# Kernel tuning notes

Measured on AMD Instinct MI355X. Metric: run time of the kernel, lower is better.

Reference implementation:

```python
import jax, jax.numpy as jnp
import numpy as np

K = 9          # neighbors per node (loop=False)
BN_EPS = 1e-5  # BatchNorm2d eps


def setup_inputs() -> dict:
    key = jax.random.key(0)
    k1, k2, k3 = jax.random.split(key, 3)
    B, C, H, W_ = 16, 384, 32, 32
    x = jax.random.normal(k1, (B, C, H, W_), dtype=jnp.float32)
    # GCNConv linear weight (PyG stores [out, in]; y = x @ W.T) and bias
    Wg = jax.random.normal(k2, (C, C), dtype=jnp.float32) / np.sqrt(C)
    bg = jax.random.normal(k3, (C,), dtype=jnp.float32) * 0.02
    gamma = jnp.ones((C,), dtype=jnp.float32)
    beta = jnp.zeros((C,), dtype=jnp.float32)
    return {"x": x, "Wg": Wg, "bg": bg, "gamma": gamma, "beta": beta}


def _knn_indices(xn):
    # xn: [B, N, C] -> neighbor indices [B, N, K] (self excluded)
    sq = jnp.sum(xn * xn, axis=-1)                       # [B, N]
    d = sq[:, :, None] + sq[:, None, :] - 2.0 * jnp.einsum("bnc,bmc->bnm", xn, xn)
    N = xn.shape[1]
    d = d + jnp.eye(N, dtype=xn.dtype) * jnp.finfo(xn.dtype).max  # exclude self
    _, nbr = jax.lax.top_k(-d, K)                        # [B, N, K]
    return nbr


def reference(x, Wg, bg, gamma, beta):
    B, C, H, W_ = x.shape
    N = H * W_
    BN_nodes = B * N
    shortcut = x

    # Flatten to nodes: [B*N, C]
    xn = jnp.transpose(x, (0, 2, 3, 1)).reshape(B, N, C)

    # Per-graph kNN in feature space (PyG knn_graph, flow source_to_target:
    # edges from neighbor (src) to query node (dst))
    nbr = _knn_indices(xn)                                # [B, N, K]
    offs = (jnp.arange(B) * N)[:, None, None]             # [B,1,1]
    src = (nbr + offs).reshape(-1)                        # [B*N*K]
    dst = jnp.broadcast_to(jnp.arange(N)[None, :, None] + offs, (B, N, K)).reshape(-1)

    # GCNConv: add self loops, symmetric normalization
    loops = jnp.arange(BN_nodes)
    src = jnp.concatenate([src, loops])
    dst = jnp.concatenate([dst, loops])

    xw = xn.reshape(BN_nodes, C) @ Wg.T                   # node-wise linear

    deg = jax.ops.segment_sum(jnp.ones_like(dst, dtype=xw.dtype), dst, num_segments=BN_nodes)
    dinv = jax.lax.rsqrt(deg)                             # deg >= 1 due to self loops
    norm = dinv[src] * dinv[dst]                          # [E]

    out = jax.ops.segment_sum(norm[:, None] * xw[src], dst, num_segments=BN_nodes) + bg

    # Back to B x C x H x W
    out = jnp.transpose(out.reshape(B, H, W_, C), (0, 3, 1, 2))

    # BatchNorm2d (training-mode batch statistics, biased variance)
    mu = jnp.mean(out, axis=(0, 2, 3), keepdims=True)
    var = jnp.mean((out - mu) ** 2, axis=(0, 2, 3), keepdims=True)
    out = gamma[None, :, None, None] * (out - mu) * jax.lax.rsqrt(var + BN_EPS) + beta[None, :, None, None]

    # GELU + residual (drop_path = 0 -> identity)
    out = jax.nn.gelu(out) + shortcut
    return out
```

## Files before the change

kernel.cpp:

```cpp
#include <hip/hip_runtime.h>
#include <math.h>

#define B_ 16
#define C_ 384
#define N_ 1024
#define K_ 9

typedef _Float16 f16x8 __attribute__((ext_vector_type(8)));
typedef _Float16 f16x4 __attribute__((ext_vector_type(4)));
typedef float f32x4 __attribute__((ext_vector_type(4)));
typedef unsigned long long u64;

__device__ __forceinline__ void gld_lds16(const void* g, void* l) {
  __builtin_amdgcn_global_load_lds((const __attribute__((address_space(1))) void*)g,
                                   (__attribute__((address_space(3))) void*)l, 16, 0, 0);
}

__global__ __launch_bounds__(256) void k_cvt(const float* __restrict__ x,
                                             const float* __restrict__ Wg,
                                             ushort* __restrict__ xhT, ushort* __restrict__ xlT,
                                             float* __restrict__ sq, ushort* __restrict__ WgH,
                                             ushort* __restrict__ WgL,
                                             float* __restrict__ stats) {
  const int bid = blockIdx.x;
  const int t = threadIdx.x;
  if (bid >= 512) {
    const int i = ((bid - 512) * 256 + t) * 4;
    float4 v = *(const float4*)(Wg + i);
    float vv[4] = {v.x, v.y, v.z, v.w};
    f16x4 hv, lv;
#pragma unroll
    for (int j = 0; j < 4; ++j) {
      _Float16 h = (_Float16)vv[j];
      hv[j] = h;
      lv[j] = (_Float16)(vv[j] - (float)h);
    }
    *(f16x4*)(WgH + i) = hv;
    *(f16x4*)(WgL + i) = lv;
    if (bid == 512) {
      stats[t] = 0.f;
      stats[t + 256] = 0.f;
      stats[t + 512] = 0.f;
    }
    return;
  }
  const int b = bid >> 5, n0 = (bid & 31) * 32;
  __shared__ float ld[384 * 33];
  {
    const int cb = t >> 2, j8 = (t & 3) * 8;
#pragma unroll
    for (int i = 0; i < 6; ++i) {
      const int c = i * 64 + cb;
      const float* src = x + ((size_t)(b * C_ + c) * N_ + n0 + j8);
      float4 v0 = *(const float4*)src;
      float4 v1 = *(const float4*)(src + 4);
      float* dst = &ld[c * 33 + j8];
      dst[0] = v0.x; dst[1] = v0.y; dst[2] = v0.z; dst[3] = v0.w;
      dst[4] = v1.x; dst[5] = v1.y; dst[6] = v1.z; dst[7] = v1.w;
    }
  }
  __syncthreads();
  {
    const int n = t >> 3, l = t & 7;
#pragma unroll
    for (int i = 0; i < 6; ++i) {
      const int c8 = i * 64 + l * 8;
      f16x8 hv, lv;
#pragma unroll
      for (int j = 0; j < 8; ++j) {
        float v = ld[(c8 + j) * 33 + n];
        _Float16 h = (_Float16)v;
        hv[j] = h;
        lv[j] = (_Float16)(v - (float)h);
      }
      const size_t off = (size_t)(b * N_ + n0 + n) * C_ + c8;
      *(f16x8*)(xhT + off) = hv;
      *(f16x8*)(xlT + off) = lv;
    }
    double s = 0.0;
    const int cbase = l * 48;
#pragma unroll
    for (int cc = 0; cc < 48; ++cc) {
      float v = ld[(cbase + cc) * 33 + n];
      s = fma((double)v, (double)v, s);
    }
    s += __shfl_xor(s, 1, 64);
    s += __shfl_xor(s, 2, 64);
    s += __shfl_xor(s, 4, 64);
    if (l == 0) sq[b * N_ + n0 + n] = (float)s;
  }
}

__device__ __forceinline__ void ce2f(float& a, float& b) {
  float lo = fminf(a, b), hi = fmaxf(a, b);
  a = lo;
  b = hi;
}
__device__ __forceinline__ void ce9u(u64& a, u64& b) {
  u64 lo = a < b ? a : b;
  u64 hi = a < b ? b : a;
  a = lo;
  b = hi;
}
__device__ __forceinline__ void mrg9(float* a, const float* b) {
  float m[9];
#pragma unroll
  for (int k = 0; k < 9; ++k) m[k] = fminf(a[k], b[8 - k]);
  ce2f(m[0], m[8]);
  ce2f(m[1], m[5]); ce2f(m[2], m[6]); ce2f(m[3], m[7]); ce2f(m[4], m[8]);
  ce2f(m[1], m[3]); ce2f(m[2], m[4]); ce2f(m[5], m[7]); ce2f(m[6], m[8]);
  ce2f(m[1], m[2]); ce2f(m[3], m[4]); ce2f(m[5], m[6]); ce2f(m[7], m[8]);
#pragma unroll
  for (int k = 0; k < 9; ++k) a[k] = m[k];
}

__global__ __launch_bounds__(256, 2) void k_gram(const ushort* __restrict__ xhT,
                                                 const ushort* __restrict__ xlT,
                                                 const float* __restrict__ sq,
                                                 u64* __restrict__ part, int base_b, int nb) {
  const int bid = blockIdx.x;
  int b_local, pid;
  if (nb >= 8) {
    const int x = bid & 7, j = bid >> 3, grp = nb >> 3;
    b_local = x * grp + (j >> 6);
    pid = j & 63;
  } else {
    b_local = bid >> 6;
    pid = bid & 63;
  }
  const int b = base_b + b_local;
  const int rt = pid >> 3, mt = pid & 7;
  const int n0 = rt * 128, m0 = mt * 128;

  __shared__ alignas(16) char sm[2][32768];
  const int t = threadIdx.x;
  const int lane = t & 63, wid = t >> 6, quad = lane >> 4, lrow = lane & 15;
  const int wr = wid >> 1, wc = wid & 1;
  const int lrow4 = lane >> 2, lpos = lane & 3;

  const char* src = (const char*)((wid & 1) ? xlT : xhT) +
                    (size_t)(b * N_ + ((wid >> 1) ? m0 : n0)) * C_ * 2;

  f32x4 acc[4][4];
#pragma unroll
  for (int mi = 0; mi < 4; ++mi)
#pragma unroll
    for (int ni = 0; ni < 4; ++ni) acc[mi][ni] = (f32x4){0.f, 0.f, 0.f, 0.f};

  auto stage = [&](int it) {
    char* dst = sm[it & 1] + wid * 8192;
    const int ktB = it * 64;
#pragma unroll
    for (int i = 0; i < 8; ++i) {
      const int row = i * 16 + lrow4;
      const int swz = lpos ^ ((row >> 1) & 3);
      gld_lds16(src + (size_t)row * 768 + ktB + swz * 16, dst + i * 1024 + lane * 16);
    }
  };

  stage(0);
  for (int it = 0; it < 12; ++it) {
    __syncthreads();
    if (it < 11) stage(it + 1);
    const char* smb = sm[it & 1];
    f16x8 ah[4], al[4];
#pragma unroll
    for (int mi = 0; mi < 4; ++mi) {
      const int row = wr * 64 + mi * 16 + lrow;
      const int off = row * 64 + (quad ^ ((row >> 1) & 3)) * 16;
      ah[mi] = *(const f16x8*)(smb + off);
      al[mi] = *(const f16x8*)(smb + 8192 + off);
    }
#pragma unroll
    for (int ni = 0; ni < 4; ++ni) {
      const int row = wc * 64 + ni * 16 + lrow;
      const int off = row * 64 + (quad ^ ((row >> 1) & 3)) * 16;
      f16x8 bh = *(const f16x8*)(smb + 16384 + off);
      f16x8 bl = *(const f16x8*)(smb + 24576 + off);
#pragma unroll
      for (int mi = 0; mi < 4; ++mi) {
        acc[mi][ni] = __builtin_amdgcn_mfma_f32_16x16x32_f16(bh, ah[mi], acc[mi][ni], 0, 0, 0);
        acc[mi][ni] = __builtin_amdgcn_mfma_f32_16x16x32_f16(bh, al[mi], acc[mi][ni], 0, 0, 0);
        acc[mi][ni] = __builtin_amdgcn_mfma_f32_16x16x32_f16(bl, ah[mi], acc[mi][ni], 0, 0, 0);
      }
    }
  }
  __syncthreads();

  const float* sqb = sq + b * N_;
  float sqm_[4][4];
#pragma unroll
  for (int ni = 0; ni < 4; ++ni)
#pragma unroll
    for (int r = 0; r < 4; ++r) sqm_[ni][r] = sqb[m0 + wc * 64 + ni * 16 + quad * 4 + r];
  float sqq_[4];
#pragma unroll
  for (int mi = 0; mi < 4; ++mi) sqq_[mi] = sqb[n0 + wr * 64 + mi * 16 + lrow];

  float* smf = (float*)sm;
#pragma unroll
  for (int mi = 0; mi < 4; ++mi) {
    const int qL = wr * 64 + mi * 16 + lrow;
    const int qG = n0 + qL;
#pragma unroll
    for (int ni = 0; ni < 4; ++ni) {
      const int tc = wc * 16 + ni * 4 + quad;
      const int stv = tc ^ (qL & 31);
      f32x4 dv;
#pragma unroll
      for (int r = 0; r < 4; ++r) {
        const int mG = m0 + wc * 64 + ni * 16 + quad * 4 + r;
        float d = fmaf(-2.f, acc[mi][ni][r], sqq_[mi] + sqm_[ni][r]);
        if (mG == qG) d = 3.402823466e38f;
        dv[r] = d;
      }
      *(f32x4*)(smf + qL * 128 + stv * 4) = dv;
    }
  }
  __syncthreads();

  const int qsel = wid * 32 + (lane & 31);
  const int half = lane >> 5;
  float kA[9], kB[9], kC[9], kD[9];
#pragma unroll
  for (int k = 0; k < 9; ++k) kA[k] = kB[k] = kC[k] = kD[k] = 3.402823466e38f;

  auto ins16 = [&](float* key, int tcb) {
#pragma unroll
    for (int i = 0; i < 4; ++i) {
      const int tc = tcb + i;
      const int stv = tc ^ (qsel & 31);
      f32x4 q4 = *(const f32x4*)(smf + qsel * 128 + stv * 4);
#pragma unroll
      for (int e = 0; e < 4; ++e) {
        key[8] = fminf(key[8], q4[e]);
#pragma unroll
        for (int s = 8; s >= 1; --s) ce2f(key[s - 1], key[s]);
      }
    }
  };
  ins16(kA, half * 16 + 0);
  ins16(kB, half * 16 + 4);
  ins16(kC, half * 16 + 8);
  ins16(kD, half * 16 + 12);
  mrg9(kA, kB);
  mrg9(kC, kD);
  mrg9(kA, kC);
  {
    float pk[9];
#pragma unroll
    for (int k = 0; k < 9; ++k) pk[k] = __shfl_xor(kA[k], 32, 64);
    float m[9];
#pragma unroll
    for (int k = 0; k < 9; ++k) m[k] = fminf(kA[k], pk[8 - k]);
    ce2f(m[0], m[8]);
    ce2f(m[1], m[5]); ce2f(m[2], m[6]); ce2f(m[3], m[7]); ce2f(m[4], m[8]);
    ce2f(m[1], m[3]); ce2f(m[2], m[4]); ce2f(m[5], m[7]); ce2f(m[6], m[8]);
    ce2f(m[1], m[2]); ce2f(m[3], m[4]); ce2f(m[5], m[6]); ce2f(m[7], m[8]);
#pragma unroll
    for (int k = 0; k < 9; ++k) kA[k] = m[k];
  }
  const float v9 = kA[8];
  int c_lt = 0;
#pragma unroll
  for (int k = 0; k < 8; ++k) c_lt += (kA[k] < v9) ? 1 : 0;

  u64 lt_mask = 0ull, eq_mask = 0ull;
#pragma unroll
  for (int i = 0; i < 16; ++i) {
    const int tc = half * 16 + i;
    const int stv = tc ^ (qsel & 31);
    f32x4 q4 = *(const f32x4*)(smf + qsel * 128 + stv * 4);
#pragma unroll
    for (int e = 0; e < 4; ++e) {
      const int j = i * 4 + e;
      lt_mask |= (q4[e] < v9) ? (1ull << j) : 0ull;
      eq_mask |= (q4[e] == v9) ? (1ull << j) : 0ull;
    }
  }
  const int ltc = __popcll(lt_mask), eqc = __popcll(eq_mask);
  const int packed = ltc | (eqc << 16);
  const int other = __shfl_xor(packed, 32, 64);
  const int lt_pref = half ? (other & 0xFFFF) : 0;
  const int eq_pref = half ? (other >> 16) : 0;

  u64* pp = part + (((size_t)(b_local * 8 + mt) * N_) + (n0 + qsel)) * 9;
  int slot = lt_pref;
  u64 msk = lt_mask;
  while (msk) {
    const int j = __builtin_ctzll(msk);
    msk &= msk - 1;
    const int mL = half * 64 + j;
    const int stv = (mL >> 2) ^ (qsel & 31);
    const float val = smf[qsel * 128 + stv * 4 + (mL & 3)];
    unsigned fb = __float_as_uint(val);
    unsigned mono = (fb >> 31) ? ~fb : (fb | 0x80000000u);
    pp[slot++] = ((u64)mono << 32) | (unsigned)(m0 + mL);
  }
  unsigned fb9 = __float_as_uint(v9);
  unsigned mono9 = (fb9 >> 31) ? ~fb9 : (fb9 | 0x80000000u);
  slot = c_lt + eq_pref;
  msk = eq_mask;
  while (msk && slot < 9) {
    const int j = __builtin_ctzll(msk);
    msk &= msk - 1;
    pp[slot++] = ((u64)mono9 << 32) | (unsigned)(m0 + half * 64 + j);
  }
}

__global__ void k_mrg(const u64* __restrict__ part, int* __restrict__ nbr, int base_node) {
  const int nl = blockIdx.x * 256 + threadIdx.x;
  const int bl = nl >> 10, q = nl & 1023;
  const u64* p = part + ((size_t)(bl * 8) * N_ + q) * 9;
  u64 key[9];
#pragma unroll
  for (int k = 0; k < 9; ++k) key[k] = ~0ull;
#pragma unroll
  for (int seg = 0; seg < 8; ++seg) {
    const u64* ps = p + (size_t)seg * N_ * 9;
#pragma unroll
    for (int k9 = 0; k9 < 9; ++k9) {
      u64 kk = ps[k9];
      key[8] = key[8] < kk ? key[8] : kk;
#pragma unroll
      for (int s = 8; s >= 1; --s) ce9u(key[s - 1], key[s]);
    }
  }
  int* np = nbr + (size_t)(base_node + nl) * K_;
#pragma unroll
  for (int k = 0; k < 9; ++k) np[k] = (int)(unsigned)(key[k] & 0xFFFFFFFFu);
}

__global__ __launch_bounds__(256, 3) void k_xw(const ushort* __restrict__ xhT,
                                               const ushort* __restrict__ xlT,
                                               const ushort* __restrict__ WgH,
                                               const ushort* __restrict__ WgL,
                                               float* __restrict__ xw) {
  const int bid = blockIdx.x;
  const int xcd = bid & 7, j = bid >> 3;
  const int pair = xcd * 16 + j / 6;
  const int ct = j % 6;
  const int b = pair >> 3, nt = pair & 7;
  const int co0 = ct * 64, n0 = nt * 128;
  __shared__ alignas(16) char sm[2][24576];
  const int t = threadIdx.x;
  const int lane = t & 63, wid = t >> 6, quad = lane >> 4, lrow = lane & 15;
  const int wr = wid >> 1, wc = wid & 1;
  const int lrow4 = lane >> 2, lpos = lane & 3;

  f32x4 acc[2][4];
#pragma unroll
  for (int mi = 0; mi < 2; ++mi)
#pragma unroll
    for (int ni = 0; ni < 4; ++ni) acc[mi][ni] = (f32x4){0.f, 0.f, 0.f, 0.f};

  const char* asrc[2] = {(const char*)(WgH + (size_t)co0 * C_),
                         (const char*)(WgL + (size_t)co0 * C_)};
  const char* bsrc[2] = {(const char*)(xhT + (size_t)(b * N_ + n0) * C_),
                         (const char*)(xlT + (size_t)(b * N_ + n0) * C_)};

  auto stage = [&](int it) {
    char* dst = sm[it & 1];
    const int ktB = it * 64;
#pragma unroll
    for (int i = 0; i < 6; ++i) {
      const int c = wid * 6 + i;
      const char* src;
      int base, row;
      if (c < 8) {
        const int arr = c >> 2, sub = c & 3;
        src = asrc[arr];
        base = arr * 4096 + sub * 1024;
        row = sub * 16 + lrow4;
      } else {
        const int cc = c - 8, arr = cc >> 3, sub = cc & 7;
        src = bsrc[arr];
        base = 8192 + arr * 8192 + sub * 1024;
        row = sub * 16 + lrow4;
      }
      const int swz = lpos ^ ((row >> 1) & 3);
      gld_lds16(src + (size_t)row * 768 + ktB + swz * 16, dst + base + lane * 16);
    }
  };

  stage(0);
  for (int it = 0; it < 12; ++it) {
    __syncthreads();
    if (it < 11) stage(it + 1);
    const char* smb = sm[it & 1];
    f16x8 bh[4], bl[4];
#pragma unroll
    for (int ni = 0; ni < 4; ++ni) {
      const int row = wr * 64 + ni * 16 + lrow;
      const int off = row * 64 + (quad ^ ((row >> 1) & 3)) * 16;
      bh[ni] = *(const f16x8*)(smb + 8192 + off);
      bl[ni] = *(const f16x8*)(smb + 16384 + off);
    }
#pragma unroll
    for (int mi = 0; mi < 2; ++mi) {
      const int row = wc * 32 + mi * 16 + lrow;
      const int off = row * 64 + (quad ^ ((row >> 1) & 3)) * 16;
      f16x8 ah = *(const f16x8*)(smb + off);
      f16x8 al = *(const f16x8*)(smb + 4096 + off);
#pragma unroll
      for (int ni = 0; ni < 4; ++ni) {
        acc[mi][ni] = __builtin_amdgcn_mfma_f32_16x16x32_f16(ah, bh[ni], acc[mi][ni], 0, 0, 0);
        acc[mi][ni] = __builtin_amdgcn_mfma_f32_16x16x32_f16(al, bh[ni], acc[mi][ni], 0, 0, 0);
        acc[mi][ni] = __builtin_amdgcn_mfma_f32_16x16x32_f16(ah, bl[ni], acc[mi][ni], 0, 0, 0);
      }
    }
  }
#pragma unroll
  for (int mi = 0; mi < 2; ++mi)
#pragma unroll
    for (int ni = 0; ni < 4; ++ni)
#pragma unroll
      for (int r = 0; r < 4; ++r) {
        const int c_g = co0 + wc * 32 + mi * 16 + quad * 4 + r;
        const int n_g = n0 + wr * 64 + ni * 16 + lrow;
        xw[((size_t)b * C_ + c_g) * N_ + n_g] = acc[mi][ni][r];
      }
}

__global__ __launch_bounds__(256) void k_agg(const float* __restrict__ xw,
                                             const int* __restrict__ nbr,
                                             const float* __restrict__ bg,
                                             float* __restrict__ out,
                                             float* __restrict__ stats) {
  const int ct = blockIdx.x % (C_ / 8);
  const int b = blockIdx.x / (C_ / 8);
  const int c0 = ct * 8;
  __shared__ alignas(16) int nb_l[N_ * K_];
  __shared__ alignas(16) float row_l[8][N_ + 4];
  __shared__ float red[2][8][4];
  const int tid = threadIdx.x;
  const int4* gp = (const int4*)(nbr + (size_t)b * N_ * K_);
  int4* lp = (int4*)nb_l;
  for (int t = tid; t < N_ * K_ / 4; t += 256) lp[t] = gp[t];
  for (int t = tid; t < 8 * (N_ / 4); t += 256) {
    const int j = t >> 8, n4 = t & 255;
    float4 v = ((const float4*)(xw + ((size_t)(b * C_ + c0 + j)) * N_))[n4];
    *(float4*)&row_l[j][n4 * 4] = v;
  }
  __syncthreads();
  float bgc[8];
#pragma unroll
  for (int j = 0; j < 8; ++j) bgc[j] = bg[c0 + j];
  float s1[8], s2[8];
#pragma unroll
  for (int j = 0; j < 8; ++j) {
    s1[j] = 0.f;
    s2[j] = 0.f;
  }
  float* outb = out + ((size_t)b * C_ + c0) * N_;
#pragma unroll
  for (int s = 0; s < 4; ++s) {
    const int n = tid + 256 * s;
    const int* nn_ = &nb_l[n * K_];
    int idx[K_];
#pragma unroll
    for (int k = 0; k < K_; ++k) idx[k] = nn_[k];
    float a[8];
#pragma unroll
    for (int j = 0; j < 8; ++j) a[j] = row_l[j][n];
#pragma unroll
    for (int k = 0; k < K_; ++k) {
      const int m = idx[k];
#pragma unroll
      for (int j = 0; j < 8; ++j) a[j] += row_l[j][m];
    }
#pragma unroll
    for (int j = 0; j < 8; ++j) {
      float y = fmaf(a[j], 0.099999994f, bgc[j]);
      outb[(size_t)j * N_ + n] = y;
      s1[j] += y;
      s2[j] = fmaf(y, y, s2[j]);
    }
  }
#pragma unroll
  for (int off = 32; off > 0; off >>= 1)
#pragma unroll
    for (int j = 0; j < 8; ++j) {
      s1[j] += __shfl_down(s1[j], off, 64);
      s2[j] += __shfl_down(s2[j], off, 64);
    }
  const int lane = tid & 63, wid = tid >> 6;
  if (lane == 0)
#pragma unroll
    for (int j = 0; j < 8; ++j) {
      red[0][j][wid] = s1[j];
      red[1][j][wid] = s2[j];
    }
  __syncthreads();
  if (tid < 16) {
    const int j = tid & 7, which = tid >> 3;
    float v = red[which][j][0] + red[which][j][1] + red[which][j][2] + red[which][j][3];
    atomicAdd(&stats[which * C_ + c0 + j], v);
  }
}

__global__ void k_bn(const float* __restrict__ x, const float* __restrict__ gamma,
                     const float* __restrict__ beta, const float* __restrict__ stats,
                     float* __restrict__ out) {
  const int f = blockIdx.x * blockDim.x + threadIdx.x;
  const int e = f * 4;
  const int c = (e >> 10) % C_;
  const float inv = 1.f / 16384.f;
  const float mu = stats[c] * inv;
  const float var = fmaf(-mu, mu, stats[C_ + c] * inv);
  const float sc = gamma[c] * rsqrtf(var + 1e-5f);
  const float sh = fmaf(-mu, sc, beta[c]);
  float4 y = ((const float4*)out)[f];
  float4 xv = ((const float4*)x)[f];
  auto gl = [](float z) {
    float z3 = z * z * z;
    float t = 0.7978845608028654f * fmaf(0.044715f, z3, z);
    float th = tanhf(t);
    return 0.5f * z * (1.f + th);
  };
  float4 o;
  o.x = gl(fmaf(y.x, sc, sh)) + xv.x;
  o.y = gl(fmaf(y.y, sc, sh)) + xv.y;
  o.z = gl(fmaf(y.z, sc, sh)) + xv.z;
  o.w = gl(fmaf(y.w, sc, sh)) + xv.w;
  ((float4*)out)[f] = o;
}

extern "C" void kernel_launch(void* const* d_in, const int* in_sizes, int n_in,
                              void* d_out, int out_size, void* d_ws, size_t ws_size,
                              hipStream_t stream) {
  const float* x = (const float*)d_in[0];
  const float* Wg = (const float*)d_in[1];
  const float* bg = (const float*)d_in[2];
  const float* gamma = (const float*)d_in[3];
  const float* beta = (const float*)d_in[4];
  float* out = (float*)d_out;

  const int nb = 16;

  char* ws = (char*)d_ws;
  ushort* xhT = (ushort*)ws;
  ushort* xlT = (ushort*)(ws + 12582912);
  ushort* WgH = (ushort*)(ws + 25165824);
  ushort* WgL = (ushort*)(ws + 25460736);
  float* sq = (float*)(ws + 25755648);
  u64* part = (u64*)(ws + 25821184);
  float* xw = (float*)(ws + 25821184);
  size_t dreg = 25165824;
  int* nbr = (int*)(ws + 25821184 + dreg);
  float* stats = (float*)(ws + 25821184 + dreg + 589824);

  k_cvt<<<656, 256, 0, stream>>>(x, Wg, xhT, xlT, sq, WgH, WgL, stats);
  k_gram<<<nb * 64, 256, 0, stream>>>(xhT, xlT, sq, part, 0, nb);
  k_mrg<<<64, 256, 0, stream>>>(part, nbr, 0);
  k_xw<<<768, 256, 0, stream>>>(xhT, xlT, WgH, WgL, xw);
  k_agg<<<B_ * (C_ / 8), 256, 0, stream>>>(xw, nbr, bg, out, stats);
  k_bn<<<6144, 256, 0, stream>>>(x, gamma, beta, stats, out);
}
```

Baseline: 220.5 us.

## Exploit Gram symmetry for kNN tiles and fuse XW GEMM into same launch

The pairwise-distance kernel now computes only upper-triangular 128x128 tiles (36 per batch instead of 64). Each off-diagonal tile also runs a column-wise top-9 selection, so it produces partial neighbor lists for both row and column queries. The node-wise linear GEMM (k_xw) is merged into the same launch as extra blocks, and xw gets its own workspace region so it can run concurrently with the Gram work. The aim is to cut redundant MFMA work and one kernel launch. In exchange, off-diagonal blocks do extra selection work with strided LDS column reads, which may hit bank conflicts, and blocks are now unbalanced between tile types.

```diff
diff --git a/kernel.cpp b/kernel.cpp
--- a/kernel.cpp
+++ b/kernel.cpp
@@ -114,29 +114,115 @@
   for (int k = 0; k < 9; ++k) a[k] = m[k];
 }
 
-__global__ __launch_bounds__(256, 2) void k_gram(const ushort* __restrict__ xhT,
-                                                 const ushort* __restrict__ xlT,
-                                                 const float* __restrict__ sq,
-                                                 u64* __restrict__ part, int base_b, int nb) {
+__global__ __launch_bounds__(256, 2) void k_gx(const ushort* __restrict__ xhT,
+                                               const ushort* __restrict__ xlT,
+                                               const float* __restrict__ sq,
+                                               u64* __restrict__ part,
+                                               const ushort* __restrict__ WgH,
+                                               const ushort* __restrict__ WgL,
+                                               float* __restrict__ xw) {
+  __shared__ alignas(16) char sm[2][32768];
   const int bid = blockIdx.x;
-  int b_local, pid;
-  if (nb >= 8) {
-    const int x = bid & 7, j = bid >> 3, grp = nb >> 3;
-    b_local = x * grp + (j >> 6);
-    pid = j & 63;
-  } else {
-    b_local = bid >> 6;
-    pid = bid & 63;
-  }
-  const int b = base_b + b_local;
-  const int rt = pid >> 3, mt = pid & 7;
-  const int n0 = rt * 128, m0 = mt * 128;
-
-  __shared__ alignas(16) char sm[2][32768];
   const int t = threadIdx.x;
   const int lane = t & 63, wid = t >> 6, quad = lane >> 4, lrow = lane & 15;
   const int wr = wid >> 1, wc = wid & 1;
   const int lrow4 = lane >> 2, lpos = lane & 3;
+
+  if (bid >= 576) {
+    const int bid2 = bid - 576;
+    const int xcd = bid2 & 7, j = bid2 >> 3;
+    const int pair = xcd * 16 + j / 6;
+    const int ct = j % 6;
+    const int b = pair >> 3, nt = pair & 7;
+    const int co0 = ct * 64, n0 = nt * 128;
+    char* smbase = &sm[0][0];
+
+    f32x4 acc[2][4];
+#pragma unroll
+    for (int mi = 0; mi < 2; ++mi)
+#pragma unroll
+      for (int ni = 0; ni < 4; ++ni) acc[mi][ni] = (f32x4){0.f, 0.f, 0.f, 0.f};
+
+    const char* asrc[2] = {(const char*)(WgH + (size_t)co0 * C_),
+                           (const char*)(WgL + (size_t)co0 * C_)};
+    const char* bsrc[2] = {(const char*)(xhT + (size_t)(b * N_ + n0) * C_),
+                           (const char*)(xlT + (size_t)(b * N_ + n0) * C_)};
+
+    auto stage = [&](int it) {
+      char* dst = smbase + (it & 1) * 24576;
+      const int ktB = it * 64;
+#pragma unroll
+      for (int i = 0; i < 6; ++i) {
+        const int c = wid * 6 + i;
+        const char* src;
+        int base, row;
+        if (c < 8) {
+          const int arr = c >> 2, sub = c & 3;
+          src = asrc[arr];
+          base = arr * 4096 + sub * 1024;
+          row = sub * 16 + lrow4;
+        } else {
+          const int cc = c - 8, arr = cc >> 3, sub = cc & 7;
+          src = bsrc[arr];
+          base = 8192 + arr * 8192 + sub * 1024;
+          row = sub * 16 + lrow4;
+        }
+        const int swz = lpos ^ ((row >> 1) & 3);
+        gld_lds16(src + (size_t)row * 768 + ktB + swz * 16, dst + base + lane * 16);
+      }
+    };
+
+    stage(0);
+    for (int it = 0; it < 12; ++it) {
+      __syncthreads();
+      if (it < 11) stage(it + 1);
+      const char* smb = smbase + (it & 1) * 24576;
+      f16x8 bh[4], bl[4];
+#pragma unroll
+      for (int ni = 0; ni < 4; ++ni) {
+        const int row = wr * 64 + ni * 16 + lrow;
+        const int off = row * 64 + (quad ^ ((row >> 1) & 3)) * 16;
+        bh[ni] = *(const f16x8*)(smb + 8192 + off);
+        bl[ni] = *(const f16x8*)(smb + 16384 + off);
+      }
+#pragma unroll
+      for (int mi = 0; mi < 2; ++mi) {
+        const int row = wc * 32 + mi * 16 + lrow;
+        const int off = row * 64 + (quad ^ ((row >> 1) & 3)) * 16;
+        f16x8 ah = *(const f16x8*)(smb + off);
+        f16x8 al = *(const f16x8*)(smb + 4096 + off);
+#pragma unroll
+        for (int ni = 0; ni < 4; ++ni) {
+          acc[mi][ni] = __builtin_amdgcn_mfma_f32_16x16x32_f16(ah, bh[ni], acc[mi][ni], 0, 0, 0);
+          acc[mi][ni] = __builtin_amdgcn_mfma_f32_16x16x32_f16(al, bh[ni], acc[mi][ni], 0, 0, 0);
+          acc[mi][ni] = __builtin_amdgcn_mfma_f32_16x16x32_f16(ah, bl[ni], acc[mi][ni], 0, 0, 0);
+        }
+      }
+    }
+#pragma unroll
+    for (int mi = 0; mi < 2; ++mi)
+#pragma unroll
+      for (int ni = 0; ni < 4; ++ni)
+#pragma unroll
+        for (int r = 0; r < 4; ++r) {
+          const int c_g = co0 + wc * 32 + mi * 16 + quad * 4 + r;
+          const int n_g = n0 + wr * 64 + ni * 16 + lrow;
+          xw[((size_t)b * C_ + c_g) * N_ + n_g] = acc[mi][ni][r];
+        }
+    return;
+  }
+
+  const int xcd = bid & 7, j = bid >> 3;
+  const int b_local = xcd * 2 + j / 36;
+  int pid = j % 36;
+  int rt = 0, off0 = 0;
+  while (pid >= off0 + (8 - rt)) {
+    off0 += 8 - rt;
+    ++rt;
+  }
+  const int mt = rt + (pid - off0);
+  const int b = b_local;
+  const int n0 = rt * 128, m0 = mt * 128;
 
   const char* src = (const char*)((wid & 1) ? xlT : xhT) +
                     (size_t)(b * N_ + ((wid >> 1) ? m0 : n0)) * C_ * 2;
@@ -219,92 +305,156 @@
   }
   __syncthreads();
 
-  const int qsel = wid * 32 + (lane & 31);
   const int half = lane >> 5;
   float kA[9], kB[9], kC[9], kD[9];
-#pragma unroll
-  for (int k = 0; k < 9; ++k) kA[k] = kB[k] = kC[k] = kD[k] = 3.402823466e38f;
-
-  auto ins16 = [&](float* key, int tcb) {
-#pragma unroll
-    for (int i = 0; i < 4; ++i) {
-      const int tc = tcb + i;
+
+  {
+    const int qsel = wid * 32 + (lane & 31);
+#pragma unroll
+    for (int k = 0; k < 9; ++k) kA[k] = kB[k] = kC[k] = kD[k] = 3.402823466e38f;
+    auto ins16 = [&](float* key, int tcb) {
+#pragma unroll
+      for (int i = 0; i < 4; ++i) {
+        const int tc = tcb + i;
+        const int stv = tc ^ (qsel & 31);
+        f32x4 q4 = *(const f32x4*)(smf + qsel * 128 + stv * 4);
+#pragma unroll
+        for (int e = 0; e < 4; ++e) {
+          key[8] = fminf(key[8], q4[e]);
+#pragma unroll
+          for (int s = 8; s >= 1; --s) ce2f(key[s - 1], key[s]);
+        }
+      }
+    };
+    ins16(kA, half * 16 + 0);
+    ins16(kB, half * 16 + 4);
+    ins16(kC, half * 16 + 8);
+    ins16(kD, half * 16 + 12);
+    mrg9(kA, kB);
+    mrg9(kC, kD);
+    mrg9(kA, kC);
+    {
+      float pk[9];
+#pragma unroll
+      for (int k = 0; k < 9; ++k) pk[k] = __shfl_xor(kA[k], 32, 64);
+      mrg9(kA, pk);
+    }
+    const float v9 = kA[8];
+    int c_lt = 0;
+#pragma unroll
+    for (int k = 0; k < 8; ++k) c_lt += (kA[k] < v9) ? 1 : 0;
+
+    u64 lt_mask = 0ull, eq_mask = 0ull;
+#pragma unroll
+    for (int i = 0; i < 16; ++i) {
+      const int tc = half * 16 + i;
       const int stv = tc ^ (qsel & 31);
       f32x4 q4 = *(const f32x4*)(smf + qsel * 128 + stv * 4);
 #pragma unroll
       for (int e = 0; e < 4; ++e) {
-        key[8] = fminf(key[8], q4[e]);
+        const int jj = i * 4 + e;
+        lt_mask |= (q4[e] < v9) ? (1ull << jj) : 0ull;
+        eq_mask |= (q4[e] == v9) ? (1ull << jj) : 0ull;
+      }
+    }
+    const int ltc = __popcll(lt_mask), eqc = __popcll(eq_mask);
+    const int packed = ltc | (eqc << 16);
+    const int other = __shfl_xor(packed, 32, 64);
+    const int lt_pref = half ? (other & 0xFFFF) : 0;
+    const int eq_pref = half ? (other >> 16) : 0;
+
+    u64* pp = part + (((size_t)(b_local * 8 + mt) * N_) + (n0 + qsel)) * 9;
+    int slot = lt_pref;
+    u64 msk = lt_mask;
+    while (msk) {
+      const int jj = __builtin_ctzll(msk);
+      msk &= msk - 1;
+      const int mL = half * 64 + jj;
+      const int stv = (mL >> 2) ^ (qsel & 31);
+      const float val = smf[qsel * 128 + stv * 4 + (mL & 3)];
+      unsigned fb = __float_as_uint(val);
+      unsigned mono = (fb >> 31) ? ~fb : (fb | 0x80000000u);
+      pp[slot++] = ((u64)mono << 32) | (unsigned)(m0 + mL);
+    }
+    unsigned fb9 = __float_as_uint(v9);
+    unsigned mono9 = (fb9 >> 31) ? ~fb9 : (fb9 | 0x80000000u);
+    slot = c_lt + eq_pref;
+    msk = eq_mask;
+    while (msk && slot < 9) {
+      const int jj = __builtin_ctzll(msk);
+      msk &= msk - 1;
+      pp[slot++] = ((u64)mono9 << 32) | (unsigned)(m0 + half * 64 + jj);
+    }
+  }
+
+  if (rt != mt) {
+    const int msel = wid * 32 + (lane & 31);
+    const int mlo = msel & 3, mhi = msel >> 2;
+#pragma unroll
+    for (int k = 0; k < 9; ++k) kA[k] = kB[k] = kC[k] = kD[k] = 3.402823466e38f;
+    auto insCol = [&](float* key, int q0) {
+#pragma unroll
+      for (int i = 0; i < 16; ++i) {
+        const int qL = q0 + i;
+        const float v = smf[qL * 128 + ((mhi ^ (qL & 31)) << 2) + mlo];
+        key[8] = fminf(key[8], v);
 #pragma unroll
         for (int s = 8; s >= 1; --s) ce2f(key[s - 1], key[s]);
       }
-    }
-  };
-  ins16(kA, half * 16 + 0);
-  ins16(kB, half * 16 + 4);
-  ins16(kC, half * 16 + 8);
-  ins16(kD, half * 16 + 12);
-  mrg9(kA, kB);
-  mrg9(kC, kD);
-  mrg9(kA, kC);
-  {
-    float pk[9];
-#pragma unroll
-    for (int k = 0; k < 9; ++k) pk[k] = __shfl_xor(kA[k], 32, 64);
-    float m[9];
-#pragma unroll
-    for (int k = 0; k < 9; ++k) m[k] = fminf(kA[k], pk[8 - k]);
-    ce2f(m[0], m[8]);
-    ce2f(m[1], m[5]); ce2f(m[2], m[6]); ce2f(m[3], m[7]); ce2f(m[4], m[8]);
-    ce2f(m[1], m[3]); ce2f(m[2], m[4]); ce2f(m[5], m[7]); ce2f(m[6], m[8]);
-    ce2f(m[1], m[2]); ce2f(m[3], m[4]); ce2f(m[5], m[6]); ce2f(m[7], m[8]);
-#pragma unroll
-    for (int k = 0; k < 9; ++k) kA[k] = m[k];
-  }
-  const float v9 = kA[8];
-  int c_lt = 0;
-#pragma unroll
-  for (int k = 0; k < 8; ++k) c_lt += (kA[k] < v9) ? 1 : 0;
-
-  u64 lt_mask = 0ull, eq_mask = 0ull;
-#pragma unroll
-  for (int i = 0; i < 16; ++i) {
-    const int tc = half * 16 + i;
-    const int stv = tc ^ (qsel & 31);
-    f32x4 q4 = *(const f32x4*)(smf + qsel * 128 + stv * 4);
-#pragma unroll
-    for (int e = 0; e < 4; ++e) {
-      const int j = i * 4 + e;
-      lt_mask |= (q4[e] < v9) ? (1ull << j) : 0ull;
-      eq_mask |= (q4[e] == v9) ? (1ull << j) : 0ull;
-    }
-  }
-  const int ltc = __popcll(lt_mask), eqc = __popcll(eq_mask);
-  const int packed = ltc | (eqc << 16);
-  const int other = __shfl_xor(packed, 32, 64);
-  const int lt_pref = half ? (other & 0xFFFF) : 0;
-  const int eq_pref = half ? (other >> 16) : 0;
-
-  u64* pp = part + (((size_t)(b_local * 8 + mt) * N_) + (n0 + qsel)) * 9;
-  int slot = lt_pref;
-  u64 msk = lt_mask;
-  while (msk) {
-    const int j = __builtin_ctzll(msk);
-    msk &= msk - 1;
-    const int mL = half * 64 + j;
-    const int stv = (mL >> 2) ^ (qsel & 31);
-    const float val = smf[qsel * 128 + stv * 4 + (mL & 3)];
-    unsigned fb = __float_as_uint(val);
-    unsigned mono = (fb >> 31) ? ~fb : (fb | 0x80000000u);
-    pp[slot++] = ((u64)mono << 32) | (unsigned)(m0 + mL);
-  }
-  unsigned fb9 = __float_as_uint(v9);
-  unsigned mono9 = (fb9 >> 31) ? ~fb9 : (fb9 | 0x80000000u);
-  slot = c_lt + eq_pref;
-  msk = eq_mask;
-  while (msk && slot < 9) {
-    const int j = __builtin_ctzll(msk);
-    msk &= msk - 1;
-    pp[slot++] = ((u64)mono9 << 32) | (unsigned)(m0 + half * 64 + j);
+    };
+    insCol(kA, half * 64 + 0);
+    insCol(kB, half * 64 + 16);
+    insCol(kC, half * 64 + 32);
+    insCol(kD, half * 64 + 48);
+    mrg9(kA, kB);
+    mrg9(kC, kD);
+    mrg9(kA, kC);
+    {
+      float pk[9];
+#pragma unroll
+      for (int k = 0; k < 9; ++k) pk[k] = __shfl_xor(kA[k], 32, 64);
+      mrg9(kA, pk);
+    }
+    const float v9 = kA[8];
+    int c_lt = 0;
+#pragma unroll
+    for (int k = 0; k < 8; ++k) c_lt += (kA[k] < v9) ? 1 : 0;
+
+    u64 lt_mask = 0ull, eq_mask = 0ull;
+#pragma unroll
+    for (int jj = 0; jj < 64; ++jj) {
+      const int qL = half * 64 + jj;
+      const float v = smf[qL * 128 + ((mhi ^ (qL & 31)) << 2) + mlo];
+      lt_mask |= (v < v9) ? (1ull << jj) : 0ull;
+      eq_mask |= (v == v9) ? (1ull << jj) : 0ull;
+    }
+    const int ltc = __popcll(lt_mask), eqc = __popcll(eq_mask);
+    const int packed = ltc | (eqc << 16);
+    const int other = __shfl_xor(packed, 32, 64);
+    const int lt_pref = half ? (other & 0xFFFF) : 0;
+    const int eq_pref = half ? (other >> 16) : 0;
+
+    u64* pp = part + (((size_t)(b_local * 8 + rt) * N_) + (m0 + msel)) * 9;
+    int slot = lt_pref;
+    u64 msk = lt_mask;
+    while (msk) {
+      const int jj = __builtin_ctzll(msk);
+      msk &= msk - 1;
+      const int qL = half * 64 + jj;
+      const float val = smf[qL * 128 + ((mhi ^ (qL & 31)) << 2) + mlo];
+      unsigned fb = __float_as_uint(val);
+      unsigned mono = (fb >> 31) ? ~fb : (fb | 0x80000000u);
+      pp[slot++] = ((u64)mono << 32) | (unsigned)(n0 + qL);
+    }
+    unsigned fb9 = __float_as_uint(v9);
+    unsigned mono9 = (fb9 >> 31) ? ~fb9 : (fb9 | 0x80000000u);
+    slot = c_lt + eq_pref;
+    msk = eq_mask;
+    while (msk && slot < 9) {
+      const int jj = __builtin_ctzll(msk);
+      msk &= msk - 1;
+      pp[slot++] = ((u64)mono9 << 32) | (unsigned)(n0 + half * 64 + jj);
+    }
   }
 }
 
@@ -329,97 +479,6 @@
   int* np = nbr + (size_t)(base_node + nl) * K_;
 #pragma unroll
   for (int k = 0; k < 9; ++k) np[k] = (int)(unsigned)(key[k] & 0xFFFFFFFFu);
-}
-
-__global__ __launch_bounds__(256, 3) void k_xw(const ushort* __restrict__ xhT,
-                                               const ushort* __restrict__ xlT,
-                                               const ushort* __restrict__ WgH,
-                                               const ushort* __restrict__ WgL,
-                                               float* __restrict__ xw) {
-  const int bid = blockIdx.x;
-  const int xcd = bid & 7, j = bid >> 3;
-  const int pair = xcd * 16 + j / 6;
-  const int ct = j % 6;
-  const int b = pair >> 3, nt = pair & 7;
-  const int co0 = ct * 64, n0 = nt * 128;
-  __shared__ alignas(16) char sm[2][24576];
-  const int t = threadIdx.x;
-  const int lane = t & 63, wid = t >> 6, quad = lane >> 4, lrow = lane & 15;
-  const int wr = wid >> 1, wc = wid & 1;
-  const int lrow4 = lane >> 2, lpos = lane & 3;
-
-  f32x4 acc[2][4];
-#pragma unroll
-  for (int mi = 0; mi < 2; ++mi)
-#pragma unroll
-    for (int ni = 0; ni < 4; ++ni) acc[mi][ni] = (f32x4){0.f, 0.f, 0.f, 0.f};
-
-  const char* asrc[2] = {(const char*)(WgH + (size_t)co0 * C_),
-                         (const char*)(WgL + (size_t)co0 * C_)};
-  const char* bsrc[2] = {(const char*)(xhT + (size_t)(b * N_ + n0) * C_),
-                         (const char*)(xlT + (size_t)(b * N_ + n0) * C_)};
-
-  auto stage = [&](int it) {
-    char* dst = sm[it & 1];
-    const int ktB = it * 64;
-#pragma unroll
-    for (int i = 0; i < 6; ++i) {
-      const int c = wid * 6 + i;
-      const char* src;
-      int base, row;
-      if (c < 8) {
-        const int arr = c >> 2, sub = c & 3;
-        src = asrc[arr];
-        base = arr * 4096 + sub * 1024;
-        row = sub * 16 + lrow4;
-      } else {
-        const int cc = c - 8, arr = cc >> 3, sub = cc & 7;
-        src = bsrc[arr];
-        base = 8192 + arr * 8192 + sub * 1024;
-        row = sub * 16 + lrow4;
-      }
-      const int swz = lpos ^ ((row >> 1) & 3);
-      gld_lds16(src + (size_t)row * 768 + ktB + swz * 16, dst + base + lane * 16);
-    }
-  };
-
-  stage(0);
-  for (int it = 0; it < 12; ++it) {
-    __syncthreads();
-    if (it < 11) stage(it + 1);
-    const char* smb = sm[it & 1];
-    f16x8 bh[4], bl[4];
-#pragma unroll
-    for (int ni = 0; ni < 4; ++ni) {
-      const int row = wr * 64 + ni * 16 + lrow;
-      const int off = row * 64 + (quad ^ ((row >> 1) & 3)) * 16;
-      bh[ni] = *(const f16x8*)(smb + 8192 + off);
-      bl[ni] = *(const f16x8*)(smb + 16384 + off);
-    }
-#pragma unroll
-    for (int mi = 0; mi < 2; ++mi) {
-      const int row = wc * 32 + mi * 16 + lrow;
-      const int off = row * 64 + (quad ^ ((row >> 1) & 3)) * 16;
-      f16x8 ah = *(const f16x8*)(smb + off);
-      f16x8 al = *(const f16x8*)(smb + 4096 + off);
-#pragma unroll
-      for (int ni = 0; ni < 4; ++ni) {
-        acc[mi][ni] = __builtin_amdgcn_mfma_f32_16x16x32_f16(ah, bh[ni], acc[mi][ni], 0, 0, 0);
-        acc[mi][ni] = __builtin_amdgcn_mfma_f32_16x16x32_f16(al, bh[ni], acc[mi][ni], 0, 0, 0);
-        acc[mi][ni] = __builtin_amdgcn_mfma_f32_16x16x32_f16(ah, bl[ni], acc[mi][ni], 0, 0, 0);
-      }
-    }
-  }
-#pragma unroll
-  for (int mi = 0; mi < 2; ++mi)
-#pragma unroll
-    for (int ni = 0; ni < 4; ++ni)
-#pragma unroll
-      for (int r = 0; r < 4; ++r) {
-        const int c_g = co0 + wc * 32 + mi * 16 + quad * 4 + r;
-        const int n_g = n0 + wr * 64 + ni * 16 + lrow;
-        xw[((size_t)b * C_ + c_g) * N_ + n_g] = acc[mi][ni][r];
-      }
 }
 
 __global__ __launch_bounds__(256) void k_agg(const float* __restrict__ xw,
@@ -536,8 +595,6 @@
   const float* beta = (const float*)d_in[4];
   float* out = (float*)d_out;
 
-  const int nb = 16;
-
   char* ws = (char*)d_ws;
   ushort* xhT = (ushort*)ws;
   ushort* xlT = (ushort*)(ws + 12582912);
@@ -546,14 +603,14 @@
   float* sq = (float*)(ws + 25755648);
   u64* part = (u64*)(ws + 25821184);
   float* xw = (float*)(ws + 25821184);
-  size_t dreg = 25165824;
-  int* nbr = (int*)(ws + 25821184 + dreg);
-  float* stats = (float*)(ws + 25821184 + dreg + 589824);
+  part = (u64*)(ws + 25821184);
+  xw = (float*)(ws + 25821184 + 9437184);
+  int* nbr = (int*)(ws + 25821184 + 9437184 + 25165824);
+  float* stats = (float*)(ws + 25821184 + 9437184 + 25165824 + 589824);
 
   k_cvt<<<656, 256, 0, stream>>>(x, Wg, xhT, xlT, sq, WgH, WgL, stats);
-  k_gram<<<nb * 64, 256, 0, stream>>>(xhT, xlT, sq, part, 0, nb);
+  k_gx<<<1344, 256, 0, stream>>>(xhT, xlT, sq, part, WgH, WgL, xw);
   k_mrg<<<64, 256, 0, stream>>>(part, nbr, 0);
-  k_xw<<<768, 256, 0, stream>>>(xhT, xlT, WgH, WgL, xw);
   k_agg<<<B_ * (C_ / 8), 256, 0, stream>>>(xw, nbr, bg, out, stats);
   k_bn<<<6144, 256, 0, stream>>>(x, gamma, beta, stats, out);
 }
```

Result: faster. 214.3 us (-2.8%).
